# Optimization experiments

Measured on AMD Instinct MI355X. Metric: run time of the kernel, lower is better.

Reference implementation:

```python
import jax, jax.numpy as jnp
import numpy as np

NEG_SLOPE = 0.2  # PyG GATConv default negative_slope
EPS = 1e-16      # PyG softmax denominator epsilon


def gat_conv(x, W, att_src, att_dst, bias, src, dst, num_nodes, concat):
    H, C = att_src.shape
    h = (x @ W).reshape(-1, H, C)                    # [N,H,C]
    a_src = jnp.einsum('nhc,hc->nh', h, att_src)      # [N,H]
    a_dst = jnp.einsum('nhc,hc->nh', h, att_dst)      # [N,H]
    e = a_src[src] + a_dst[dst]                       # [E,H]
    e = jax.nn.leaky_relu(e, NEG_SLOPE)
    # segment softmax over incoming edges of each destination node
    e_max = jax.ops.segment_max(e, dst, num_segments=num_nodes)   # [N,H]
    e_max = jnp.where(jnp.isfinite(e_max), e_max, 0.0)
    p = jnp.exp(e - e_max[dst])                        # [E,H]
    denom = jax.ops.segment_sum(p, dst, num_segments=num_nodes)   # [N,H]
    alpha = p / (denom[dst] + EPS)                     # [E,H]
    msg = h[src] * alpha[:, :, None]                   # [E,H,C]
    out = jax.ops.segment_sum(msg, dst, num_segments=num_nodes)   # [N,H,C]
    if concat:
        out = out.reshape(num_nodes, H * C)
    else:
        out = out.mean(axis=1)
    return out + bias


def setup_inputs() -> dict:
    key = jax.random.key(0)
    ks = jax.random.split(key, 10)
    N, E, Fin, H, C, OUT = 50000, 400000, 128, 8, 32, 32
    s = 0.05
    return {
        'x': jax.random.normal(ks[0], (N, Fin), jnp.float32),
        'edge_index': jax.random.randint(ks[1], (2, E), 0, N, jnp.int64),
        'W1': jax.random.normal(ks[2], (Fin, H * C), jnp.float32) * s,
        'att_src1': jax.random.normal(ks[3], (H, C), jnp.float32) * s,
        'att_dst1': jax.random.normal(ks[4], (H, C), jnp.float32) * s,
        'b1': jax.random.normal(ks[5], (H * C,), jnp.float32) * s,
        'W2': jax.random.normal(ks[6], (H * C, H * OUT), jnp.float32) * s,
        'att_src2': jax.random.normal(ks[7], (H, OUT), jnp.float32) * s,
        'att_dst2': jax.random.normal(ks[8], (H, OUT), jnp.float32) * s,
        'b2': jax.random.normal(ks[9], (OUT,), jnp.float32) * s,
    }


def reference(x, edge_index, W1, att_src1, att_dst1, b1, W2, att_src2, att_dst2, b2):
    N = x.shape[0]
    src, dst = edge_index[0], edge_index[1]
    h = gat_conv(x, W1, att_src1, att_dst1, b1, src, dst, N, concat=True)
    h = jax.nn.elu(h)  # dropout p=0 / eval: identity
    out = gat_conv(h, W2, att_src2, att_dst2, b2, src, dst, N, concat=False)
    return out
```

## Files before the change

kernel.cpp:

```cpp
#include <hip/hip_runtime.h>
#include <math.h>

#define NEG_SLOPE 0.2f

typedef float f32x4 __attribute__((ext_vector_type(4)));
typedef short bf16x8 __attribute__((ext_vector_type(8)));
typedef unsigned short ushortv8 __attribute__((ext_vector_type(8)));

__device__ __forceinline__ unsigned short f2bf(float f) {
    union { float f; unsigned u; } uu; uu.f = f;
    unsigned r = uu.u + 0x7FFF + ((uu.u >> 16) & 1);
    return (unsigned short)(r >> 16);
}
__device__ __forceinline__ float bf2f(unsigned short u) {
    union { unsigned u; float f; } x; x.u = ((unsigned)u) << 16; return x.f;
}

__global__ void prep_kernel(const float* __restrict__ x, unsigned short* __restrict__ xb,
                            const float* __restrict__ W1, unsigned short* __restrict__ Wt1,
                            const float* __restrict__ W2, unsigned short* __restrict__ Wt2,
                            int* __restrict__ counts, int* __restrict__ cursor,
                            int n4x, int N)
{
    int t = blockIdx.x * 256 + threadIdx.x;
    if (t < n4x) {
        float4 v = ((const float4*)x)[t];
        ushort4 o;
        o.x = f2bf(v.x); o.y = f2bf(v.y); o.z = f2bf(v.z); o.w = f2bf(v.w);
        ((ushort4*)xb)[t] = o;
        return;
    }
    int u = t - n4x;
    if (u < 32768) {
        int nn = u >> 7, k = u & 127;
        Wt1[u] = f2bf(W1[(size_t)k * 256 + nn]);
        return;
    }
    u -= 32768;
    if (u < 65536) {
        int nn = u >> 8, k = u & 255;
        Wt2[u] = f2bf(W2[(size_t)k * 256 + nn]);
        return;
    }
    u -= 65536;
    if (u < N) { counts[u] = 0; cursor[u] = 0; }
}

__global__ void hist_kernel(const int* __restrict__ dst, int* __restrict__ counts, int E)
{
    int e = blockIdx.x * 256 + threadIdx.x;
    if (e < E) atomicAdd(&counts[dst[e]], 1);
}

__global__ __launch_bounds__(256) void gemm_mfma(
    const unsigned short* __restrict__ A,
    const unsigned short* __restrict__ Bt,
    unsigned short* __restrict__ C,
    int M, int K)
{
    __shared__ unsigned short As[128 * 64];
    __shared__ unsigned short Bs[128 * 64];
    const int tid  = threadIdx.x;
    const int lane = tid & 63;
    const int wave = tid >> 6;
    const int wr = wave >> 1, wc = wave & 1;
    const int row0 = blockIdx.x * 128;
    const int col0 = blockIdx.y * 128;

    f32x4 acc[4][4] = {};

    for (int k0 = 0; k0 < K; k0 += 64) {
        ushortv8 va[4], vb[4];
        #pragma unroll
        for (int i = 0; i < 4; ++i) {
            int c  = i * 256 + tid;
            int r  = c >> 3, cc = c & 7;
            int ga = row0 + r; if (ga >= M) ga = M - 1;
            va[i] = *(const ushortv8*)(A  + (size_t)ga * K + k0 + cc * 8);
            vb[i] = *(const ushortv8*)(Bt + (size_t)(col0 + r) * K + k0 + cc * 8);
        }
        __syncthreads();
        #pragma unroll
        for (int i = 0; i < 4; ++i) {
            int c  = i * 256 + tid;
            int r  = c >> 3, cc = c & 7;
            int sl = cc ^ (r & 7);
            *(ushortv8*)(As + r * 64 + sl * 8) = va[i];
            *(ushortv8*)(Bs + r * 64 + sl * 8) = vb[i];
        }
        __syncthreads();

        #pragma unroll
        for (int kk = 0; kk < 2; ++kk) {
            const int kbyte = kk * 64 + ((lane >> 4) << 4);
            bf16x8 af[4], bfr[4];
            #pragma unroll
            for (int m = 0; m < 4; ++m) {
                int r = wr * 64 + m * 16 + (lane & 15);
                af[m] = *(const bf16x8*)((const char*)As + r * 128 + (kbyte ^ ((r & 7) << 4)));
            }
            #pragma unroll
            for (int n = 0; n < 4; ++n) {
                int r = wc * 64 + n * 16 + (lane & 15);
                bfr[n] = *(const bf16x8*)((const char*)Bs + r * 128 + (kbyte ^ ((r & 7) << 4)));
            }
            #pragma unroll
            for (int m = 0; m < 4; ++m)
                #pragma unroll
                for (int n = 0; n < 4; ++n)
                    acc[m][n] = __builtin_amdgcn_mfma_f32_16x16x32_bf16(
                        af[m], bfr[n], acc[m][n], 0, 0, 0);
        }
        __syncthreads();
    }

    #pragma unroll
    for (int m = 0; m < 4; ++m) {
        int rbase = row0 + wr * 64 + m * 16 + ((lane >> 4) << 2);
        #pragma unroll
        for (int j = 0; j < 4; ++j) {
            int grow = rbase + j;
            if (grow < M) {
                #pragma unroll
                for (int n = 0; n < 4; ++n)
                    C[(size_t)grow * 256 + col0 + wc * 64 + n * 16 + (lane & 15)] =
                        f2bf(acc[m][n][j]);
            }
        }
    }
}

__global__ void att_kernel(const unsigned short* __restrict__ h,
                           const float* __restrict__ att_s,
                           const float* __restrict__ att_d,
                           float* __restrict__ a_s, float* __restrict__ a_d, int N)
{
    int t = blockIdx.x * 256 + threadIdx.x;
    if (t >= N * 8) return;
    int n = t >> 3, hh = t & 7;
    const ushortv8* hp = (const ushortv8*)(h + (size_t)n * 256 + hh * 32);
    const float*    ap = att_s + hh * 32;
    const float*    bp = att_d + hh * 32;
    float ss = 0.f, dd = 0.f;
    #pragma unroll
    for (int i = 0; i < 4; ++i) {
        ushortv8 hv = hp[i];
        #pragma unroll
        for (int q = 0; q < 8; ++q) {
            float f = bf2f(hv[q]);
            ss += f * ap[i*8 + q];
            dd += f * bp[i*8 + q];
        }
    }
    a_s[t] = ss; a_d[t] = dd;
}

__global__ __launch_bounds__(256) void scan_blk(
    const int* __restrict__ counts, int* __restrict__ incl, int* __restrict__ bsum, int N)
{
    __shared__ int wtot[4], wexc[4];
    int t = blockIdx.x * 256 + threadIdx.x;
    int lane = threadIdx.x & 63, wid = threadIdx.x >> 6;
    int v = (t < N) ? counts[t] : 0;
    int s = v;
    #pragma unroll
    for (int off = 1; off < 64; off <<= 1) {
        int u = __shfl_up(s, off);
        if (lane >= off) s += u;
    }
    if (lane == 63) wtot[wid] = s;
    __syncthreads();
    if (threadIdx.x == 0) {
        int r = 0;
        #pragma unroll
        for (int w = 0; w < 4; ++w) { wexc[w] = r; r += wtot[w]; }
    }
    __syncthreads();
    int out = s + wexc[wid];
    if (t < N) incl[t] = out;
    if (threadIdx.x == 255) bsum[blockIdx.x] = out;
}

__global__ __launch_bounds__(256) void scan_top(int* __restrict__ bsum, int nb)
{
    __shared__ int wtot[4], wexc[4];
    int tid = threadIdx.x;
    int lane = tid & 63, wid = tid >> 6;
    int v = (tid < nb) ? bsum[tid] : 0;
    int s = v;
    #pragma unroll
    for (int off = 1; off < 64; off <<= 1) {
        int u = __shfl_up(s, off);
        if (lane >= off) s += u;
    }
    if (lane == 63) wtot[wid] = s;
    __syncthreads();
    if (tid == 0) {
        int r = 0;
        #pragma unroll
        for (int w = 0; w < 4; ++w) { wexc[w] = r; r += wtot[w]; }
    }
    __syncthreads();
    if (tid < nb) bsum[tid] = s + wexc[wid] - v;
}

__global__ void fill_kernel(const int* __restrict__ src, const int* __restrict__ dst,
                            const int* __restrict__ incl, const int* __restrict__ bsum,
                            int* __restrict__ rowptr, int* __restrict__ cursor,
                            int* __restrict__ esrc, int N, int E)
{
    int t = blockIdx.x * 256 + threadIdx.x;
    if (t < N) {
        rowptr[t + 1] = incl[t] + bsum[t >> 8];
        if (t == 0) rowptr[0] = 0;
    }
    if (t < E) {
        int d = dst[t];
        int rp = bsum[d >> 8] + ((d & 255) ? incl[d - 1] : 0);
        int pos = rp + atomicAdd(&cursor[d], 1);
        esrc[pos] = src[t];
    }
}

template<int LAYER>
__global__ __launch_bounds__(256) void gat_agg(
    const unsigned short* __restrict__ h, const float* __restrict__ a_s,
    const float* __restrict__ a_d, const int* __restrict__ rowptr,
    const int* __restrict__ esrc, const float* __restrict__ bias,
    float* __restrict__ out, unsigned short* __restrict__ out_b, int N)
{
    int n = blockIdx.x * 4 + (threadIdx.x >> 6);
    if (n >= N) return;
    const int lane = threadIdx.x & 63;
    const int half = lane >> 5;
    const int sl   = lane & 31;
    const int head = sl >> 2;
    int beg = rowptr[n];
    int deg = rowptr[n + 1] - beg;

    if (deg == 0) {
        if (LAYER == 1) {
            if (half == 0) {
                ushortv8 o;
                #pragma unroll
                for (int q = 0; q < 8; ++q) {
                    float b = bias[sl*8 + q];
                    o[q] = f2bf(b > 0.f ? b : expf(b) - 1.f);
                }
                *(ushortv8*)(out_b + (size_t)n*256 + sl*8) = o;
            }
        } else {
            if (lane < 4) {
                #pragma unroll
                for (int q = 0; q < 8; ++q)
                    out[(size_t)n*32 + lane*8 + q] = bias[lane*8 + q];
            }
        }
        return;
    }

    float adn = a_d[(size_t)n*8 + head];
    float dsum = 0.f;
    float acc[8] = {0.f,0.f,0.f,0.f,0.f,0.f,0.f,0.f};

    int j0 = 0;
    for (; j0 + 8 <= deg; j0 += 8) {
        int sv[4];
        #pragma unroll
        for (int k = 0; k < 4; ++k) sv[k] = esrc[beg + j0 + 2*k + half];
        float av[4];
        #pragma unroll
        for (int k = 0; k < 4; ++k) av[k] = a_s[(size_t)sv[k]*8 + head];
        ushortv8 hv[4];
        #pragma unroll
        for (int k = 0; k < 4; ++k)
            hv[k] = *(const ushortv8*)(h + (size_t)sv[k]*256 + sl*8);
        #pragma unroll
        for (int k = 0; k < 4; ++k) {
            float e = av[k] + adn;
            e = (e > 0.f) ? e : NEG_SLOPE * e;
            float p = __expf(e);
            dsum += p;
            #pragma unroll
            for (int q = 0; q < 8; ++q) acc[q] += p * bf2f(hv[k][q]);
        }
    }
    for (; j0 + 2 <= deg; j0 += 2) {
        int s = esrc[beg + j0 + half];
        float e = a_s[(size_t)s*8 + head] + adn;
        e = (e > 0.f) ? e : NEG_SLOPE * e;
        float p = __expf(e);
        dsum += p;
        ushortv8 hv = *(const ushortv8*)(h + (size_t)s*256 + sl*8);
        #pragma unroll
        for (int q = 0; q < 8; ++q) acc[q] += p * bf2f(hv[q]);
    }
    if (j0 < deg) {
        int s = esrc[beg + j0];
        if (half == 0) {
            float e = a_s[(size_t)s*8 + head] + adn;
            e = (e > 0.f) ? e : NEG_SLOPE * e;
            float p = __expf(e);
            dsum += p;
            ushortv8 hv = *(const ushortv8*)(h + (size_t)s*256 + sl*8);
            #pragma unroll
            for (int q = 0; q < 8; ++q) acc[q] += p * bf2f(hv[q]);
        }
    }

    dsum += __shfl_xor(dsum, 32);
    #pragma unroll
    for (int q = 0; q < 8; ++q) acc[q] += __shfl_xor(acc[q], 32);
    float invd = 1.f / (dsum + 1e-16f);

    if (LAYER == 1) {
        if (half == 0) {
            ushortv8 o;
            #pragma unroll
            for (int q = 0; q < 8; ++q) {
                float val = acc[q] * invd + bias[sl*8 + q];
                o[q] = f2bf(val > 0.f ? val : expf(val) - 1.f);
            }
            *(ushortv8*)(out_b + (size_t)n*256 + sl*8) = o;
        }
    } else {
        #pragma unroll
        for (int q = 0; q < 8; ++q) acc[q] *= invd;
        #pragma unroll
        for (int m = 4; m <= 16; m <<= 1)
            #pragma unroll
            for (int q = 0; q < 8; ++q) acc[q] += __shfl_xor(acc[q], m);
        if (lane < 4) {
            float4 lo = make_float4(acc[0]*0.125f + bias[lane*8+0],
                                    acc[1]*0.125f + bias[lane*8+1],
                                    acc[2]*0.125f + bias[lane*8+2],
                                    acc[3]*0.125f + bias[lane*8+3]);
            float4 hi = make_float4(acc[4]*0.125f + bias[lane*8+4],
                                    acc[5]*0.125f + bias[lane*8+5],
                                    acc[6]*0.125f + bias[lane*8+6],
                                    acc[7]*0.125f + bias[lane*8+7]);
            *(float4*)(out + (size_t)n*32 + lane*8)     = lo;
            *(float4*)(out + (size_t)n*32 + lane*8 + 4) = hi;
        }
    }
}

extern "C" void kernel_launch(void* const* d_in, const int* in_sizes, int n_in,
                              void* d_out, int out_size, void* d_ws, size_t ws_size,
                              hipStream_t stream)
{
    const float* x   = (const float*)d_in[0];
    const int*   ei  = (const int*)  d_in[1];
    const float* W1  = (const float*)d_in[2];
    const float* as1 = (const float*)d_in[3];
    const float* ad1 = (const float*)d_in[4];
    const float* b1  = (const float*)d_in[5];
    const float* W2  = (const float*)d_in[6];
    const float* as2 = (const float*)d_in[7];
    const float* ad2 = (const float*)d_in[8];
    const float* b2  = (const float*)d_in[9];

    const int N = in_sizes[0] / 128;
    const int E = in_sizes[1] / 2;
    const int* srcp = ei;
    const int* dstp = ei + E;

    char* ws = (char*)d_ws;
    unsigned short* hb    = (unsigned short*)ws;  ws += (size_t)N * 256 * 2;
    unsigned short* xb    = (unsigned short*)ws;  ws += (size_t)N * 128 * 2;
    unsigned short* out1b = (unsigned short*)ws;  ws += (size_t)N * 256 * 2;
    unsigned short* Wt1   = (unsigned short*)ws;  ws += 256 * 128 * 2;
    unsigned short* Wt2   = (unsigned short*)ws;  ws += 256 * 256 * 2;
    float*          a_s   = (float*)ws;           ws += (size_t)N * 8 * 4;
    float*          a_d   = (float*)ws;           ws += (size_t)N * 8 * 4;
    int*            counts= (int*)ws;             ws += (size_t)N * 4;
    int*            cursor= (int*)ws;             ws += (size_t)N * 4;
    int*            incl  = (int*)ws;             ws += (size_t)N * 4;
    int*            bsum  = (int*)ws;             ws += 256 * 4;
    int*            rowptr= (int*)ws;             ws += (size_t)(N + 1) * 4;
    int*            esrc  = (int*)ws;

    const int nb  = (N + 255) / 256;
    const int n4x = N * 32;

    {
        int tot = n4x + 32768 + 65536 + N;
        prep_kernel<<<(tot + 255) / 256, 256, 0, stream>>>(
            x, xb, W1, Wt1, W2, Wt2, counts, cursor, n4x, N);
    }
    hist_kernel<<<(E + 255) / 256, 256, 0, stream>>>(dstp, counts, E);
    scan_blk<<<nb, 256, 0, stream>>>(counts, incl, bsum, N);
    scan_top<<<1, 256, 0, stream>>>(bsum, nb);
    fill_kernel<<<(E + 255) / 256, 256, 0, stream>>>(srcp, dstp, incl, bsum,
                                                     rowptr, cursor, esrc, N, E);

    const int gridM = (N + 127) / 128;

    gemm_mfma<<<dim3(gridM, 2), 256, 0, stream>>>(xb, Wt1, hb, N, 128);
    att_kernel<<<(N * 8 + 255) / 256, 256, 0, stream>>>(hb, as1, ad1, a_s, a_d, N);
    gat_agg<1><<<(N + 3) / 4, 256, 0, stream>>>(hb, a_s, a_d, rowptr, esrc, b1,
                                                nullptr, out1b, N);

    gemm_mfma<<<dim3(gridM, 2), 256, 0, stream>>>(out1b, Wt2, hb, N, 256);
    att_kernel<<<(N * 8 + 255) / 256, 256, 0, stream>>>(hb, as2, ad2, a_s, a_d, N);
    gat_agg<2><<<(N + 3) / 4, 256, 0, stream>>>(hb, a_s, a_d, rowptr, esrc, b2,
                                                (float*)d_out, nullptr, N);
}
```

Before: 204.4 us.

## Split each node's channels across two waves with four edge slots per wave

```diff
diff --git a/kernel.cpp b/kernel.cpp
--- a/kernel.cpp
+++ b/kernel.cpp
@@ -229,118 +229,106 @@
     const int* __restrict__ esrc, const float* __restrict__ bias,
     float* __restrict__ out, unsigned short* __restrict__ out_b, int N)
 {
-    int n = blockIdx.x * 4 + (threadIdx.x >> 6);
-    if (n >= N) return;
-    const int lane = threadIdx.x & 63;
-    const int half = lane >> 5;
-    const int sl   = lane & 31;
-    const int head = sl >> 2;
-    int beg = rowptr[n];
-    int deg = rowptr[n + 1] - beg;
-
-    if (deg == 0) {
-        if (LAYER == 1) {
-            if (half == 0) {
-                ushortv8 o;
-                #pragma unroll
-                for (int q = 0; q < 8; ++q) {
-                    float b = bias[sl*8 + q];
-                    o[q] = f2bf(b > 0.f ? b : expf(b) - 1.f);
-                }
-                *(ushortv8*)(out_b + (size_t)n*256 + sl*8) = o;
-            }
-        } else {
-            if (lane < 4) {
-                #pragma unroll
-                for (int q = 0; q < 8; ++q)
-                    out[(size_t)n*32 + lane*8 + q] = bias[lane*8 + q];
-            }
-        }
-        return;
-    }
-
-    float adn = a_d[(size_t)n*8 + head];
+    __shared__ float lred[2][2][32];
+    const int nslot = threadIdx.x >> 7;
+    const int wh    = (threadIdx.x >> 6) & 1;
+    const int lane  = threadIdx.x & 63;
+    const int slot  = lane >> 4;
+    const int sl    = lane & 15;
+    const int head  = wh * 4 + (sl >> 2);
+    const int n     = blockIdx.x * 2 + nslot;
+    const int chb   = wh * 128 + sl * 8;
+
     float dsum = 0.f;
     float acc[8] = {0.f,0.f,0.f,0.f,0.f,0.f,0.f,0.f};
 
-    int j0 = 0;
-    for (; j0 + 8 <= deg; j0 += 8) {
-        int sv[4];
-        #pragma unroll
-        for (int k = 0; k < 4; ++k) sv[k] = esrc[beg + j0 + 2*k + half];
-        float av[4];
-        #pragma unroll
-        for (int k = 0; k < 4; ++k) av[k] = a_s[(size_t)sv[k]*8 + head];
-        ushortv8 hv[4];
-        #pragma unroll
-        for (int k = 0; k < 4; ++k)
-            hv[k] = *(const ushortv8*)(h + (size_t)sv[k]*256 + sl*8);
-        #pragma unroll
-        for (int k = 0; k < 4; ++k) {
-            float e = av[k] + adn;
-            e = (e > 0.f) ? e : NEG_SLOPE * e;
-            float p = __expf(e);
-            dsum += p;
-            #pragma unroll
-            for (int q = 0; q < 8; ++q) acc[q] += p * bf2f(hv[k][q]);
-        }
-    }
-    for (; j0 + 2 <= deg; j0 += 2) {
-        int s = esrc[beg + j0 + half];
-        float e = a_s[(size_t)s*8 + head] + adn;
-        e = (e > 0.f) ? e : NEG_SLOPE * e;
-        float p = __expf(e);
-        dsum += p;
-        ushortv8 hv = *(const ushortv8*)(h + (size_t)s*256 + sl*8);
-        #pragma unroll
-        for (int q = 0; q < 8; ++q) acc[q] += p * bf2f(hv[q]);
-    }
-    if (j0 < deg) {
-        int s = esrc[beg + j0];
-        if (half == 0) {
+    if (n < N) {
+        const int beg = rowptr[n];
+        const int deg = rowptr[n + 1] - beg;
+        const float adn = a_d[(size_t)n*8 + head];
+
+        int j0 = 0;
+        for (; j0 + 8 <= deg; j0 += 8) {
+            #pragma unroll
+            for (int u = 0; u < 2; ++u) {
+                int s = esrc[beg + j0 + u*4 + slot];
+                float e = a_s[(size_t)s*8 + head] + adn;
+                e = (e > 0.f) ? e : NEG_SLOPE * e;
+                float p = __expf(e);
+                dsum += p;
+                ushortv8 hv = *(const ushortv8*)(h + (size_t)s*256 + chb);
+                #pragma unroll
+                for (int q = 0; q < 8; ++q) acc[q] += p * bf2f(hv[q]);
+            }
+        }
+        if (j0 + 4 <= deg) {
+            int s = esrc[beg + j0 + slot];
             float e = a_s[(size_t)s*8 + head] + adn;
             e = (e > 0.f) ? e : NEG_SLOPE * e;
             float p = __expf(e);
             dsum += p;
-            ushortv8 hv = *(const ushortv8*)(h + (size_t)s*256 + sl*8);
+            ushortv8 hv = *(const ushortv8*)(h + (size_t)s*256 + chb);
             #pragma unroll
             for (int q = 0; q < 8; ++q) acc[q] += p * bf2f(hv[q]);
-        }
-    }
-
-    dsum += __shfl_xor(dsum, 32);
-    #pragma unroll
-    for (int q = 0; q < 8; ++q) acc[q] += __shfl_xor(acc[q], 32);
-    float invd = 1.f / (dsum + 1e-16f);
-
-    if (LAYER == 1) {
-        if (half == 0) {
-            ushortv8 o;
+            j0 += 4;
+        }
+        {
+            int r = deg - j0;
+            if (slot < r) {
+                int s = esrc[beg + j0 + slot];
+                float e = a_s[(size_t)s*8 + head] + adn;
+                e = (e > 0.f) ? e : NEG_SLOPE * e;
+                float p = __expf(e);
+                dsum += p;
+                ushortv8 hv = *(const ushortv8*)(h + (size_t)s*256 + chb);
+                #pragma unroll
+                for (int q = 0; q < 8; ++q) acc[q] += p * bf2f(hv[q]);
+            }
+        }
+
+        dsum += __shfl_xor(dsum, 16);
+        dsum += __shfl_xor(dsum, 32);
+        #pragma unroll
+        for (int q = 0; q < 8; ++q) {
+            acc[q] += __shfl_xor(acc[q], 16);
+            acc[q] += __shfl_xor(acc[q], 32);
+        }
+        float invd = 1.f / (dsum + 1e-16f);
+
+        if (LAYER == 1) {
+            if (slot == 0) {
+                ushortv8 o;
+                #pragma unroll
+                for (int q = 0; q < 8; ++q) {
+                    float val = acc[q] * invd + bias[chb + q];
+                    o[q] = f2bf(val > 0.f ? val : (expf(val) - 1.f));
+                }
+                *(ushortv8*)(out_b + (size_t)n*256 + chb) = o;
+            }
+        } else {
+            #pragma unroll
+            for (int q = 0; q < 8; ++q) acc[q] *= invd;
             #pragma unroll
             for (int q = 0; q < 8; ++q) {
-                float val = acc[q] * invd + bias[sl*8 + q];
-                o[q] = f2bf(val > 0.f ? val : expf(val) - 1.f);
-            }
-            *(ushortv8*)(out_b + (size_t)n*256 + sl*8) = o;
-        }
-    } else {
-        #pragma unroll
-        for (int q = 0; q < 8; ++q) acc[q] *= invd;
-        #pragma unroll
-        for (int m = 4; m <= 16; m <<= 1)
-            #pragma unroll
-            for (int q = 0; q < 8; ++q) acc[q] += __shfl_xor(acc[q], m);
-        if (lane < 4) {
-            float4 lo = make_float4(acc[0]*0.125f + bias[lane*8+0],
-                                    acc[1]*0.125f + bias[lane*8+1],
-                                    acc[2]*0.125f + bias[lane*8+2],
-                                    acc[3]*0.125f + bias[lane*8+3]);
-            float4 hi = make_float4(acc[4]*0.125f + bias[lane*8+4],
-                                    acc[5]*0.125f + bias[lane*8+5],
-                                    acc[6]*0.125f + bias[lane*8+6],
-                                    acc[7]*0.125f + bias[lane*8+7]);
-            *(float4*)(out + (size_t)n*32 + lane*8)     = lo;
-            *(float4*)(out + (size_t)n*32 + lane*8 + 4) = hi;
+                acc[q] += __shfl_xor(acc[q], 4);
+                acc[q] += __shfl_xor(acc[q], 8);
+            }
+            if (slot == 0 && sl < 4) {
+                #pragma unroll
+                for (int q = 0; q < 8; ++q) lred[nslot][wh][sl*8 + q] = acc[q];
+            }
+        }
+    }
+
+    if (LAYER == 2) {
+        __syncthreads();
+        int t = threadIdx.x;
+        if (t < 64) {
+            int nn = blockIdx.x * 2 + (t >> 5);
+            int c = t & 31;
+            if (nn < N)
+                out[(size_t)nn*32 + c] =
+                    (lred[t>>5][0][c] + lred[t>>5][1][c]) * 0.125f + bias[c];
         }
     }
 }
@@ -395,14 +383,15 @@
                                                      rowptr, cursor, esrc, N, E);
 
     const int gridM = (N + 127) / 128;
+    const int gridAgg = (N + 1) / 2;
 
     gemm_mfma<<<dim3(gridM, 2), 256, 0, stream>>>(xb, Wt1, hb, N, 128);
     att_kernel<<<(N * 8 + 255) / 256, 256, 0, stream>>>(hb, as1, ad1, a_s, a_d, N);
-    gat_agg<1><<<(N + 3) / 4, 256, 0, stream>>>(hb, a_s, a_d, rowptr, esrc, b1,
-                                                nullptr, out1b, N);
+    gat_agg<1><<<gridAgg, 256, 0, stream>>>(hb, a_s, a_d, rowptr, esrc, b1,
+                                            nullptr, out1b, N);
 
     gemm_mfma<<<dim3(gridM, 2), 256, 0, stream>>>(out1b, Wt2, hb, N, 256);
     att_kernel<<<(N * 8 + 255) / 256, 256, 0, stream>>>(hb, as2, ad2, a_s, a_d, N);
-    gat_agg<2><<<(N + 3) / 4, 256, 0, stream>>>(hb, a_s, a_d, rowptr, esrc, b2,
-                                                (float*)d_out, nullptr, N);
-}
+    gat_agg<2><<<gridAgg, 256, 0, stream>>>(hb, a_s, a_d, rowptr, esrc, b2,
+                                            (float*)d_out, nullptr, N);
+}
```

Measured after the change: 222.4 us. 1.09x slower.
